# Performance work log

Hardware: AMD Instinct MI355X
Metric: run time of the kernel (lower is better)

Reference implementation:

```python
import jax, jax.numpy as jnp
import numpy as np

N = 50000
E = 800000
IN_FT = 256
OUT_FT = 64


def setup_inputs() -> dict:
    key = jax.random.key(0)
    k_seq, k_w, k_src, k_dst, k_val = jax.random.split(key, 5)
    seq = jax.random.normal(k_seq, (N, IN_FT), dtype=jnp.float32)
    # xavier_uniform_ for fc.weight [out_ft, in_ft]
    limit = float(np.sqrt(6.0 / (IN_FT + OUT_FT)))
    W = jax.random.uniform(k_w, (OUT_FT, IN_FT), minval=-limit, maxval=limit, dtype=jnp.float32)
    bias = jnp.zeros((OUT_FT,), dtype=jnp.float32)          # bias.data.fill_(0.0)
    alpha = jnp.full((1,), 0.25, dtype=jnp.float32)         # PReLU default init
    edge_src = jax.random.randint(k_src, (E,), 0, N, dtype=jnp.int32)
    edge_dst = jax.random.randint(k_dst, (E,), 0, N, dtype=jnp.int32)
    edge_val = jax.random.uniform(k_val, (E,), dtype=jnp.float32)
    return {"seq": seq, "W": W, "bias": bias, "alpha": alpha,
            "edge_src": edge_src, "edge_dst": edge_dst, "edge_val": edge_val}


def reference(seq, W, bias, alpha, edge_src, edge_dst, edge_val):
    # fc(seq): [N, in_ft] @ [in_ft, out_ft] -> [N, out_ft]
    fts = jnp.einsum('ni,oi->no', seq, W)
    # spmm(adj, fts): gather source features, scale by edge value, scatter-add to dst
    msgs = fts[edge_src] * edge_val[:, None]                # [E, out_ft]
    out = jax.ops.segment_sum(msgs, edge_dst, num_segments=seq.shape[0])
    out = out + bias
    # PReLU with scalar (single-channel) alpha
    return jnp.where(out >= 0, out, alpha * out)
```

## Files before the change

kernel.cpp:

```cpp
#include <hip/hip_runtime.h>
#include <hip/hip_fp16.h>

#define IN_FT 256
#define OUT_FT 64

constexpr int BIN_LOG   = 6;
constexpr int BIN_NODES = 1 << BIN_LOG;
constexpr int MAX_NBIN  = 1024;
constexpr int BIN_CAP   = 1536;
constexpr int SC_BLOCKS = 256;

constexpr float FXS  = 2097152.0f;
constexpr float IFXS = 1.0f / 2097152.0f;

typedef _Float16 half8 __attribute__((ext_vector_type(8)));
typedef float    f32x4 __attribute__((ext_vector_type(4)));

__global__ __launch_bounds__(256) void count_wconv(
    const float* __restrict__ W, half8* __restrict__ Wh,
    const int* __restrict__ dst, int* __restrict__ cnt, int E, int NBIN)
{
    const int t = (int)threadIdx.x;

    if ((int)blockIdx.x >= SC_BLOCKS) {
        int item = ((int)blockIdx.x - SC_BLOCKS) * 256 + t;
        int l  = item & 63;
        int kc = (item >> 6) & 7;
        int nt = item >> 9;
        int m  = l & 15;
        int q  = l >> 4;
        const float* wp = W + (size_t)(nt * 16 + m) * IN_FT + kc * 32 + q * 8;
        float4 w0 = *(const float4*)wp;
        float4 w1 = *(const float4*)(wp + 4);
        half8 hh;
        hh[0] = (_Float16)w0.x; hh[1] = (_Float16)w0.y;
        hh[2] = (_Float16)w0.z; hh[3] = (_Float16)w0.w;
        hh[4] = (_Float16)w1.x; hh[5] = (_Float16)w1.y;
        hh[6] = (_Float16)w1.z; hh[7] = (_Float16)w1.w;
        Wh[item] = hh;
        return;
    }

    __shared__ int h[MAX_NBIN];
    const int sb = (int)blockIdx.x;
    for (int i = t; i < NBIN; i += 256) h[i] = 0;
    __syncthreads();
    const int chunk = (E + SC_BLOCKS - 1) / SC_BLOCKS;
    const int s0 = sb * chunk;
    const int e0 = min(s0 + chunk, E);
    int i = s0 + t;
    for (; i + 768 < e0; i += 1024) {
        int d[4];
#pragma unroll
        for (int k = 0; k < 4; ++k) d[k] = dst[i + k * 256];
        __builtin_amdgcn_sched_barrier(0);
#pragma unroll
        for (int k = 0; k < 4; ++k) atomicAdd(&h[d[k] >> BIN_LOG], 1);
    }
    for (; i < e0; i += 256) atomicAdd(&h[dst[i] >> BIN_LOG], 1);
    __syncthreads();
    for (int b = t; b < NBIN; b += 256)
        cnt[(size_t)b * SC_BLOCKS + sb] = h[b];
}

__global__ __launch_bounds__(256) void scan_kernel(
    const int* __restrict__ cnt, int* __restrict__ offT,
    int* __restrict__ binTot)
{
    __shared__ int wsum[4];
    const int b    = (int)blockIdx.x;
    const int t    = (int)threadIdx.x;
    const int lane = t & 63;
    const int wv   = t >> 6;

    int c = cnt[(size_t)b * SC_BLOCKS + t];
    int incl = c;
#pragma unroll
    for (int d = 1; d < 64; d <<= 1) {
        int u = __shfl_up(incl, d, 64);
        if (lane >= d) incl += u;
    }
    if (lane == 63) wsum[wv] = incl;
    __syncthreads();
    int woff = 0;
#pragma unroll
    for (int w = 0; w < 4; ++w) if (w < wv) woff += wsum[w];
    int excl = woff + incl - c;
    offT[(size_t)t * MAX_NBIN + b] = excl;
    if (t == 255) binTot[b] = excl + c;
}

__global__ __launch_bounds__(256, 4) void fused_gemm_scatter(
    const float* __restrict__ seq, const half8* __restrict__ WhG,
    __half* __restrict__ fts, int N, int G,
    const int* __restrict__ src, const int* __restrict__ dst,
    const float* __restrict__ val, const int* __restrict__ offT,
    int2* __restrict__ binned, int E, int NBIN)
{
    __shared__ alignas(16) char smem[32768];
    const int t = (int)threadIdx.x;

    if ((int)blockIdx.x < SC_BLOCKS) {
        int* h = (int*)smem;
        const int sb = (int)blockIdx.x;
        for (int b = t; b < NBIN; b += 256)
            h[b] = offT[(size_t)sb * MAX_NBIN + b];
        __syncthreads();
        const int chunk = (E + SC_BLOCKS - 1) / SC_BLOCKS;
        const int s0 = sb * chunk;
        const int e0 = min(s0 + chunk, E);

        int i = s0 + t;
        for (; i + 768 < e0; i += 1024) {
            int d[4], s[4]; float v[4];
#pragma unroll
            for (int k = 0; k < 4; ++k) {
                d[k] = dst[i + k * 256];
                s[k] = src[i + k * 256];
                v[k] = val[i + k * 256];
            }
            __builtin_amdgcn_sched_barrier(0);
#pragma unroll
            for (int k = 0; k < 4; ++k) {
                int b = d[k] >> BIN_LOG;
                int pos = atomicAdd(&h[b], 1);
                if (pos < BIN_CAP) {
                    int2 pr;
                    pr.x = s[k] | ((d[k] & (BIN_NODES - 1)) << 16);
                    pr.y = __float_as_int(v[k] * FXS);
                    binned[(size_t)b * BIN_CAP + pos] = pr;
                }
            }
        }
        for (; i < e0; i += 256) {
            int d = dst[i];
            int b = d >> BIN_LOG;
            int pos = atomicAdd(&h[b], 1);
            if (pos < BIN_CAP) {
                int2 pr;
                pr.x = src[i] | ((d & (BIN_NODES - 1)) << 16);
                pr.y = __float_as_int(val[i] * FXS);
                binned[(size_t)b * BIN_CAP + pos] = pr;
            }
        }
        return;
    }

    const int wave = t >> 6;
    const int l    = t & 63;
    int nodeBase = ((int)blockIdx.x - SC_BLOCKS) * 64 + wave * 16;
    const bool active = (nodeBase < N);
    if (nodeBase > N - 16) nodeBase = N - 16;
    const int m = l & 15;
    const int q = l >> 4;
    const float* ap = seq + (size_t)(nodeBase + m) * IN_FT + q * 8;

    float4 A[16];
#pragma unroll
    for (int kc = 0; kc < 8; ++kc) {
        A[2 * kc]     = *(const float4*)(ap + kc * 32);
        A[2 * kc + 1] = *(const float4*)(ap + kc * 32 + 4);
    }
    {
        const int4* wg  = (const int4*)WhG;
        int4*       bsw = (int4*)smem;
#pragma unroll
        for (int i = 0; i < 8; ++i) bsw[i * 256 + t] = wg[i * 256 + t];
    }
    __syncthreads();
    const half8* Bs = (const half8*)smem;

    f32x4 acc0 = {0.f, 0.f, 0.f, 0.f};
    f32x4 acc1 = {0.f, 0.f, 0.f, 0.f};
    f32x4 acc2 = {0.f, 0.f, 0.f, 0.f};
    f32x4 acc3 = {0.f, 0.f, 0.f, 0.f};

#pragma unroll
    for (int kc = 0; kc < 8; ++kc) {
        float4 c0 = A[2 * kc], c1 = A[2 * kc + 1];
        half8 af;
        af[0] = (_Float16)c0.x; af[1] = (_Float16)c0.y;
        af[2] = (_Float16)c0.z; af[3] = (_Float16)c0.w;
        af[4] = (_Float16)c1.x; af[5] = (_Float16)c1.y;
        af[6] = (_Float16)c1.z; af[7] = (_Float16)c1.w;

        half8 b0 = Bs[(0 * 8 + kc) * 64 + l];
        half8 b1 = Bs[(1 * 8 + kc) * 64 + l];
        half8 b2 = Bs[(2 * 8 + kc) * 64 + l];
        half8 b3 = Bs[(3 * 8 + kc) * 64 + l];
        acc0 = __builtin_amdgcn_mfma_f32_16x16x32_f16(af, b0, acc0, 0, 0, 0);
        acc1 = __builtin_amdgcn_mfma_f32_16x16x32_f16(af, b1, acc1, 0, 0, 0);
        acc2 = __builtin_amdgcn_mfma_f32_16x16x32_f16(af, b2, acc2, 0, 0, 0);
        acc3 = __builtin_amdgcn_mfma_f32_16x16x32_f16(af, b3, acc3, 0, 0, 0);
    }

    if (active) {
#pragma unroll
        for (int r = 0; r < 4; ++r) {
            int node = nodeBase + q * 4 + r;
            __half* op = fts + (size_t)node * OUT_FT + m;
            op[0]  = __float2half(acc0[r]);
            op[16] = __float2half(acc1[r]);
            op[32] = __float2half(acc2[r]);
            op[48] = __float2half(acc3[r]);
        }
    }
}

__global__ __launch_bounds__(512, 4) void bin_reduce(
    const int2* __restrict__ binned, const int* __restrict__ binTot,
    const __half* __restrict__ fts, const float* __restrict__ bias,
    const float* __restrict__ alpha, float* __restrict__ out, int N)
{
    __shared__ int accum[BIN_NODES * OUT_FT];
    const int b    = (int)blockIdx.x;
    const int t    = (int)threadIdx.x;
    const int lane = t & 63;
    const int wv   = t >> 6;

    int4* a4 = (int4*)accum;
#pragma unroll
    for (int i = 0; i < (BIN_NODES * OUT_FT / 4) / 512; ++i)
        a4[i * 512 + t] = make_int4(0, 0, 0, 0);
    __syncthreads();

    const int nrec = min(binTot[b], BIN_CAP);
    const int2* rec = binned + (size_t)b * BIN_CAP;
    const unsigned short* ftsu = (const unsigned short*)fts + lane;

    int i = wv * 16;
    for (; i + 16 <= nrec; i += 8 * 16) {
        int2 pr[16];
#pragma unroll
        for (int k = 0; k < 16; ++k) pr[k] = rec[i + k];
        __builtin_amdgcn_sched_barrier(0);
        unsigned short h[16];
#pragma unroll
        for (int k = 0; k < 16; ++k)
            h[k] = ftsu[(size_t)(pr[k].x & 0xFFFF) * OUT_FT];
        __builtin_amdgcn_sched_barrier(0);
#pragma unroll
        for (int k = 0; k < 16; ++k) {
            float p = __half2float(__ushort_as_half(h[k])) * __int_as_float(pr[k].y);
            atomicAdd(&accum[(pr[k].x >> 16) * OUT_FT + lane], __float2int_rn(p));
        }
    }
    for (; i < nrec; ++i) {
        int2 pr = rec[i];
        float fv = __half2float(__ushort_as_half(ftsu[(size_t)(pr.x & 0xFFFF) * OUT_FT]));
        atomicAdd(&accum[(pr.x >> 16) * OUT_FT + lane],
                  __float2int_rn(fv * __int_as_float(pr.y)));
    }
    __syncthreads();

    const float a = alpha[0];
    for (int j = t; j < BIN_NODES * (OUT_FT / 4); j += 512) {
        int row  = j >> 4;
        int cc   = (j & 15) << 2;
        int node = (b << BIN_LOG) + row;
        if (node < N) {
            int4 v = *(int4*)&accum[row * OUT_FT + cc];
            float4 o;
            float x0 = (float)v.x * IFXS + bias[cc + 0];
            float x1 = (float)v.y * IFXS + bias[cc + 1];
            float x2 = (float)v.z * IFXS + bias[cc + 2];
            float x3 = (float)v.w * IFXS + bias[cc + 3];
            o.x = (x0 >= 0.f) ? x0 : a * x0;
            o.y = (x1 >= 0.f) ? x1 : a * x1;
            o.z = (x2 >= 0.f) ? x2 : a * x2;
            o.w = (x3 >= 0.f) ? x3 : a * x3;
            *(float4*)(out + (size_t)node * OUT_FT + cc) = o;
        }
    }
}

extern "C" void kernel_launch(void* const* d_in, const int* in_sizes, int n_in,
                              void* d_out, int out_size, void* d_ws, size_t ws_size,
                              hipStream_t stream) {
    const float* seq      = (const float*)d_in[0];
    const float* W        = (const float*)d_in[1];
    const float* bias     = (const float*)d_in[2];
    const float* alpha    = (const float*)d_in[3];
    const int*   edge_src = (const int*)d_in[4];
    const int*   edge_dst = (const int*)d_in[5];
    const float* edge_val = (const float*)d_in[6];
    float* out = (float*)d_out;

    const int N    = in_sizes[0] / IN_FT;
    const int E    = in_sizes[4];
    const int NBIN = (N + BIN_NODES - 1) >> BIN_LOG;

    size_t off = 0;
    auto take = [&](size_t bytes) -> char* {
        char* p = (char*)d_ws + off;
        off += (bytes + 255) & ~(size_t)255;
        return p;
    };
    __half* fts    = (__half*)take((size_t)N * OUT_FT * sizeof(__half));
    half8*  Wh     = (half8*)take((size_t)4 * 8 * 64 * sizeof(half8));
    int*    cnt    = (int*)take((size_t)NBIN * SC_BLOCKS * sizeof(int));
    int*    offT   = (int*)take((size_t)SC_BLOCKS * MAX_NBIN * sizeof(int));
    int*    binTot = (int*)take((size_t)NBIN * sizeof(int));
    int2*   binned = (int2*)take((size_t)NBIN * BIN_CAP * sizeof(int2));
    (void)ws_size;

    count_wconv<<<SC_BLOCKS + 8, 256, 0, stream>>>(W, Wh, edge_dst, cnt, E, NBIN);

    scan_kernel<<<NBIN, 256, 0, stream>>>(cnt, offT, binTot);

    const int G = (N + 63) / 64;
    fused_gemm_scatter<<<SC_BLOCKS + G, 256, 0, stream>>>(
        seq, Wh, fts, N, G, edge_src, edge_dst, edge_val,
        offT, binned, E, NBIN);

    bin_reduce<<<NBIN, 512, 0, stream>>>(
        binned, binTot, fts, bias, alpha, out, N);
}
```

Measured before the change: 157.4 us.

## Move GEMM into count kernel with multi-tile double-buffered loads

New measurement: 161.9 us. +2.9%, slower.

```diff
diff --git a/kernel.cpp b/kernel.cpp
--- a/kernel.cpp
+++ b/kernel.cpp
@@ -9,6 +9,7 @@
 constexpr int MAX_NBIN  = 1024;
 constexpr int BIN_CAP   = 1536;
 constexpr int SC_BLOCKS = 256;
+constexpr int TPB       = 4;
 
 constexpr float FXS  = 2097152.0f;
 constexpr float IFXS = 1.0f / 2097152.0f;
@@ -16,20 +17,45 @@
 typedef _Float16 half8 __attribute__((ext_vector_type(8)));
 typedef float    f32x4 __attribute__((ext_vector_type(4)));
 
-__global__ __launch_bounds__(256) void count_wconv(
-    const float* __restrict__ W, half8* __restrict__ Wh,
-    const int* __restrict__ dst, int* __restrict__ cnt, int E, int NBIN)
+__global__ __launch_bounds__(256, 4) void count_gemm(
+    const float* __restrict__ seq, const float* __restrict__ W,
+    __half* __restrict__ fts, const int* __restrict__ dst,
+    int* __restrict__ cnt, int N, int E, int NBIN, int TILES)
 {
+    __shared__ alignas(16) char smem[32768];
     const int t = (int)threadIdx.x;
 
-    if ((int)blockIdx.x >= SC_BLOCKS) {
-        int item = ((int)blockIdx.x - SC_BLOCKS) * 256 + t;
-        int l  = item & 63;
-        int kc = (item >> 6) & 7;
-        int nt = item >> 9;
-        int m  = l & 15;
-        int q  = l >> 4;
-        const float* wp = W + (size_t)(nt * 16 + m) * IN_FT + kc * 32 + q * 8;
+    if ((int)blockIdx.x < SC_BLOCKS) {
+        int* h = (int*)smem;
+        const int sb = (int)blockIdx.x;
+        for (int i = t; i < NBIN; i += 256) h[i] = 0;
+        __syncthreads();
+        const int chunk = (E + SC_BLOCKS - 1) / SC_BLOCKS;
+        const int s0 = sb * chunk;
+        const int e0 = min(s0 + chunk, E);
+        int i = s0 + t;
+        for (; i + 768 < e0; i += 1024) {
+            int d[4];
+#pragma unroll
+            for (int k = 0; k < 4; ++k) d[k] = dst[i + k * 256];
+            __builtin_amdgcn_sched_barrier(0);
+#pragma unroll
+            for (int k = 0; k < 4; ++k) atomicAdd(&h[d[k] >> BIN_LOG], 1);
+        }
+        for (; i < e0; i += 256) atomicAdd(&h[dst[i] >> BIN_LOG], 1);
+        __syncthreads();
+        for (int b = t; b < NBIN; b += 256)
+            cnt[(size_t)b * SC_BLOCKS + sb] = h[b];
+        return;
+    }
+
+    half8* Bs = (half8*)smem;
+#pragma unroll
+    for (int it = 0; it < 8; ++it) {
+        int item = it * 256 + t;
+        int l2 = item & 63, kc = (item >> 6) & 7, nt = item >> 9;
+        int mm = l2 & 15, qq = l2 >> 4;
+        const float* wp = W + (size_t)(nt * 16 + mm) * IN_FT + kc * 32 + qq * 8;
         float4 w0 = *(const float4*)wp;
         float4 w1 = *(const float4*)(wp + 4);
         half8 hh;
@@ -37,30 +63,111 @@
         hh[2] = (_Float16)w0.z; hh[3] = (_Float16)w0.w;
         hh[4] = (_Float16)w1.x; hh[5] = (_Float16)w1.y;
         hh[6] = (_Float16)w1.z; hh[7] = (_Float16)w1.w;
-        Wh[item] = hh;
-        return;
-    }
-
-    __shared__ int h[MAX_NBIN];
-    const int sb = (int)blockIdx.x;
-    for (int i = t; i < NBIN; i += 256) h[i] = 0;
-    __syncthreads();
-    const int chunk = (E + SC_BLOCKS - 1) / SC_BLOCKS;
-    const int s0 = sb * chunk;
-    const int e0 = min(s0 + chunk, E);
-    int i = s0 + t;
-    for (; i + 768 < e0; i += 1024) {
-        int d[4];
-#pragma unroll
-        for (int k = 0; k < 4; ++k) d[k] = dst[i + k * 256];
-        __builtin_amdgcn_sched_barrier(0);
-#pragma unroll
-        for (int k = 0; k < 4; ++k) atomicAdd(&h[d[k] >> BIN_LOG], 1);
-    }
-    for (; i < e0; i += 256) atomicAdd(&h[dst[i] >> BIN_LOG], 1);
-    __syncthreads();
-    for (int b = t; b < NBIN; b += 256)
-        cnt[(size_t)b * SC_BLOCKS + sb] = h[b];
+        Bs[item] = hh;
+    }
+    __syncthreads();
+
+    const int gb    = (int)blockIdx.x - SC_BLOCKS;
+    const int wv    = t >> 6;
+    const int l     = t & 63;
+    const int m     = l & 15;
+    const int q     = l >> 4;
+    const int tile0 = gb * TPB;
+    const int ntl   = min(TPB, TILES - tile0);
+    if (ntl <= 0) return;
+
+    f32x4 acc0 = {0.f,0.f,0.f,0.f}, acc1 = {0.f,0.f,0.f,0.f};
+    f32x4 acc2 = {0.f,0.f,0.f,0.f}, acc3 = {0.f,0.f,0.f,0.f};
+
+    auto issue = [&](float4* b, int s) {
+        const int tile = tile0 + (s >> 1);
+        const int hh = s & 1;
+        const float* ap = seq + (size_t)(tile * 64 + wv * 16 + m) * IN_FT
+                              + hh * 128 + q * 8;
+#pragma unroll
+        for (int kc = 0; kc < 4; ++kc) {
+            b[2 * kc]     = *(const float4*)(ap + kc * 32);
+            b[2 * kc + 1] = *(const float4*)(ap + kc * 32 + 4);
+        }
+    };
+    auto consume = [&](const float4* b, int hh) {
+#pragma unroll
+        for (int kc = 0; kc < 4; ++kc) {
+            float4 c0 = b[2 * kc], c1 = b[2 * kc + 1];
+            half8 af;
+            af[0] = (_Float16)c0.x; af[1] = (_Float16)c0.y;
+            af[2] = (_Float16)c0.z; af[3] = (_Float16)c0.w;
+            af[4] = (_Float16)c1.x; af[5] = (_Float16)c1.y;
+            af[6] = (_Float16)c1.z; af[7] = (_Float16)c1.w;
+            const int kg = hh * 4 + kc;
+            half8 b0 = Bs[(0 * 8 + kg) * 64 + l];
+            half8 b1 = Bs[(1 * 8 + kg) * 64 + l];
+            half8 b2 = Bs[(2 * 8 + kg) * 64 + l];
+            half8 b3 = Bs[(3 * 8 + kg) * 64 + l];
+            acc0 = __builtin_amdgcn_mfma_f32_16x16x32_f16(af, b0, acc0, 0, 0, 0);
+            acc1 = __builtin_amdgcn_mfma_f32_16x16x32_f16(af, b1, acc1, 0, 0, 0);
+            acc2 = __builtin_amdgcn_mfma_f32_16x16x32_f16(af, b2, acc2, 0, 0, 0);
+            acc3 = __builtin_amdgcn_mfma_f32_16x16x32_f16(af, b3, acc3, 0, 0, 0);
+        }
+    };
+    auto flush = [&](int ti) {
+        int nb = (tile0 + ti) * 64 + wv * 16;
+#pragma unroll
+        for (int r = 0; r < 4; ++r) {
+            int node = nb + q * 4 + r;
+            __half* op = fts + (size_t)node * OUT_FT + m;
+            op[0]  = __float2half(acc0[r]);
+            op[16] = __float2half(acc1[r]);
+            op[32] = __float2half(acc2[r]);
+            op[48] = __float2half(acc3[r]);
+        }
+        acc0 = (f32x4){0.f,0.f,0.f,0.f}; acc1 = (f32x4){0.f,0.f,0.f,0.f};
+        acc2 = (f32x4){0.f,0.f,0.f,0.f}; acc3 = (f32x4){0.f,0.f,0.f,0.f};
+    };
+
+    if (ntl == TPB) {
+        float4 bufA[8], bufB[8];
+        issue(bufA, 0);
+#pragma unroll
+        for (int s = 0; s < 2 * TPB; ++s) {
+            float4*       nxt = (s & 1) ? bufA : bufB;
+            const float4* cur = (s & 1) ? bufB : bufA;
+            if (s + 1 < 2 * TPB) issue(nxt, s + 1);
+            __builtin_amdgcn_sched_barrier(0);
+            asm volatile("" ::: "memory");
+            consume(cur, s & 1);
+            if (s & 1) flush(s >> 1);
+        }
+    } else {
+        for (int ti = 0; ti < ntl; ++ti) {
+            int tile = tile0 + ti;
+            int nb = tile * 64 + wv * 16;
+            const bool active = (nb < N);
+            if (nb > N - 16) nb = N - 16;
+            const float* ap = seq + (size_t)(nb + m) * IN_FT + q * 8;
+            float4 A[16];
+#pragma unroll
+            for (int kc = 0; kc < 8; ++kc) {
+                A[2 * kc]     = *(const float4*)(ap + kc * 32);
+                A[2 * kc + 1] = *(const float4*)(ap + kc * 32 + 4);
+            }
+            acc0 = (f32x4){0.f,0.f,0.f,0.f}; acc1 = (f32x4){0.f,0.f,0.f,0.f};
+            acc2 = (f32x4){0.f,0.f,0.f,0.f}; acc3 = (f32x4){0.f,0.f,0.f,0.f};
+#pragma unroll
+            for (int hh = 0; hh < 2; ++hh) consume(&A[hh * 8], hh);
+            if (active) {
+#pragma unroll
+                for (int r = 0; r < 4; ++r) {
+                    int node = nb + q * 4 + r;
+                    __half* op = fts + (size_t)node * OUT_FT + m;
+                    op[0]  = __float2half(acc0[r]);
+                    op[16] = __float2half(acc1[r]);
+                    op[32] = __float2half(acc2[r]);
+                    op[48] = __float2half(acc3[r]);
+                }
+            }
+        }
+    }
 }
 
 __global__ __launch_bounds__(256) void scan_kernel(
@@ -90,119 +197,52 @@
     if (t == 255) binTot[b] = excl + c;
 }
 
-__global__ __launch_bounds__(256, 4) void fused_gemm_scatter(
-    const float* __restrict__ seq, const half8* __restrict__ WhG,
-    __half* __restrict__ fts, int N, int G,
+__global__ __launch_bounds__(256) void place_kernel(
     const int* __restrict__ src, const int* __restrict__ dst,
     const float* __restrict__ val, const int* __restrict__ offT,
     int2* __restrict__ binned, int E, int NBIN)
 {
-    __shared__ alignas(16) char smem[32768];
-    const int t = (int)threadIdx.x;
-
-    if ((int)blockIdx.x < SC_BLOCKS) {
-        int* h = (int*)smem;
-        const int sb = (int)blockIdx.x;
-        for (int b = t; b < NBIN; b += 256)
-            h[b] = offT[(size_t)sb * MAX_NBIN + b];
-        __syncthreads();
-        const int chunk = (E + SC_BLOCKS - 1) / SC_BLOCKS;
-        const int s0 = sb * chunk;
-        const int e0 = min(s0 + chunk, E);
-
-        int i = s0 + t;
-        for (; i + 768 < e0; i += 1024) {
-            int d[4], s[4]; float v[4];
-#pragma unroll
-            for (int k = 0; k < 4; ++k) {
-                d[k] = dst[i + k * 256];
-                s[k] = src[i + k * 256];
-                v[k] = val[i + k * 256];
-            }
-            __builtin_amdgcn_sched_barrier(0);
-#pragma unroll
-            for (int k = 0; k < 4; ++k) {
-                int b = d[k] >> BIN_LOG;
-                int pos = atomicAdd(&h[b], 1);
-                if (pos < BIN_CAP) {
-                    int2 pr;
-                    pr.x = s[k] | ((d[k] & (BIN_NODES - 1)) << 16);
-                    pr.y = __float_as_int(v[k] * FXS);
-                    binned[(size_t)b * BIN_CAP + pos] = pr;
-                }
-            }
-        }
-        for (; i < e0; i += 256) {
-            int d = dst[i];
-            int b = d >> BIN_LOG;
+    __shared__ int h[MAX_NBIN];
+    const int t  = (int)threadIdx.x;
+    const int sb = (int)blockIdx.x;
+    for (int b = t; b < NBIN; b += 256)
+        h[b] = offT[(size_t)sb * MAX_NBIN + b];
+    __syncthreads();
+    const int chunk = (E + SC_BLOCKS - 1) / SC_BLOCKS;
+    const int s0 = sb * chunk;
+    const int e0 = min(s0 + chunk, E);
+
+    int i = s0 + t;
+    for (; i + 768 < e0; i += 1024) {
+        int d[4], s[4]; float v[4];
+#pragma unroll
+        for (int k = 0; k < 4; ++k) {
+            d[k] = dst[i + k * 256];
+            s[k] = src[i + k * 256];
+            v[k] = val[i + k * 256];
+        }
+        __builtin_amdgcn_sched_barrier(0);
+#pragma unroll
+        for (int k = 0; k < 4; ++k) {
+            int b = d[k] >> BIN_LOG;
             int pos = atomicAdd(&h[b], 1);
             if (pos < BIN_CAP) {
                 int2 pr;
-                pr.x = src[i] | ((d & (BIN_NODES - 1)) << 16);
-                pr.y = __float_as_int(val[i] * FXS);
+                pr.x = s[k] | ((d[k] & (BIN_NODES - 1)) << 16);
+                pr.y = __float_as_int(v[k] * FXS);
                 binned[(size_t)b * BIN_CAP + pos] = pr;
             }
         }
-        return;
-    }
-
-    const int wave = t >> 6;
-    const int l    = t & 63;
-    int nodeBase = ((int)blockIdx.x - SC_BLOCKS) * 64 + wave * 16;
-    const bool active = (nodeBase < N);
-    if (nodeBase > N - 16) nodeBase = N - 16;
-    const int m = l & 15;
-    const int q = l >> 4;
-    const float* ap = seq + (size_t)(nodeBase + m) * IN_FT + q * 8;
-
-    float4 A[16];
-#pragma unroll
-    for (int kc = 0; kc < 8; ++kc) {
-        A[2 * kc]     = *(const float4*)(ap + kc * 32);
-        A[2 * kc + 1] = *(const float4*)(ap + kc * 32 + 4);
-    }
-    {
-        const int4* wg  = (const int4*)WhG;
-        int4*       bsw = (int4*)smem;
-#pragma unroll
-        for (int i = 0; i < 8; ++i) bsw[i * 256 + t] = wg[i * 256 + t];
-    }
-    __syncthreads();
-    const half8* Bs = (const half8*)smem;
-
-    f32x4 acc0 = {0.f, 0.f, 0.f, 0.f};
-    f32x4 acc1 = {0.f, 0.f, 0.f, 0.f};
-    f32x4 acc2 = {0.f, 0.f, 0.f, 0.f};
-    f32x4 acc3 = {0.f, 0.f, 0.f, 0.f};
-
-#pragma unroll
-    for (int kc = 0; kc < 8; ++kc) {
-        float4 c0 = A[2 * kc], c1 = A[2 * kc + 1];
-        half8 af;
-        af[0] = (_Float16)c0.x; af[1] = (_Float16)c0.y;
-        af[2] = (_Float16)c0.z; af[3] = (_Float16)c0.w;
-        af[4] = (_Float16)c1.x; af[5] = (_Float16)c1.y;
-        af[6] = (_Float16)c1.z; af[7] = (_Float16)c1.w;
-
-        half8 b0 = Bs[(0 * 8 + kc) * 64 + l];
-        half8 b1 = Bs[(1 * 8 + kc) * 64 + l];
-        half8 b2 = Bs[(2 * 8 + kc) * 64 + l];
-        half8 b3 = Bs[(3 * 8 + kc) * 64 + l];
-        acc0 = __builtin_amdgcn_mfma_f32_16x16x32_f16(af, b0, acc0, 0, 0, 0);
-        acc1 = __builtin_amdgcn_mfma_f32_16x16x32_f16(af, b1, acc1, 0, 0, 0);
-        acc2 = __builtin_amdgcn_mfma_f32_16x16x32_f16(af, b2, acc2, 0, 0, 0);
-        acc3 = __builtin_amdgcn_mfma_f32_16x16x32_f16(af, b3, acc3, 0, 0, 0);
-    }
-
-    if (active) {
-#pragma unroll
-        for (int r = 0; r < 4; ++r) {
-            int node = nodeBase + q * 4 + r;
-            __half* op = fts + (size_t)node * OUT_FT + m;
-            op[0]  = __float2half(acc0[r]);
-            op[16] = __float2half(acc1[r]);
-            op[32] = __float2half(acc2[r]);
-            op[48] = __float2half(acc3[r]);
+    }
+    for (; i < e0; i += 256) {
+        int d = dst[i];
+        int b = d >> BIN_LOG;
+        int pos = atomicAdd(&h[b], 1);
+        if (pos < BIN_CAP) {
+            int2 pr;
+            pr.x = src[i] | ((d & (BIN_NODES - 1)) << 16);
+            pr.y = __float_as_int(val[i] * FXS);
+            binned[(size_t)b * BIN_CAP + pos] = pr;
         }
     }
 }
@@ -286,9 +326,11 @@
     const float* edge_val = (const float*)d_in[6];
     float* out = (float*)d_out;
 
-    const int N    = in_sizes[0] / IN_FT;
-    const int E    = in_sizes[4];
-    const int NBIN = (N + BIN_NODES - 1) >> BIN_LOG;
+    const int N     = in_sizes[0] / IN_FT;
+    const int E     = in_sizes[4];
+    const int NBIN  = (N + BIN_NODES - 1) >> BIN_LOG;
+    const int TILES = (N + 63) / 64;
+    const int GB    = (TILES + TPB - 1) / TPB;
 
     size_t off = 0;
     auto take = [&](size_t bytes) -> char* {
@@ -297,21 +339,19 @@
         return p;
     };
     __half* fts    = (__half*)take((size_t)N * OUT_FT * sizeof(__half));
-    half8*  Wh     = (half8*)take((size_t)4 * 8 * 64 * sizeof(half8));
     int*    cnt    = (int*)take((size_t)NBIN * SC_BLOCKS * sizeof(int));
     int*    offT   = (int*)take((size_t)SC_BLOCKS * MAX_NBIN * sizeof(int));
     int*    binTot = (int*)take((size_t)NBIN * sizeof(int));
     int2*   binned = (int2*)take((size_t)NBIN * BIN_CAP * sizeof(int2));
     (void)ws_size;
 
-    count_wconv<<<SC_BLOCKS + 8, 256, 0, stream>>>(W, Wh, edge_dst, cnt, E, NBIN);
+    count_gemm<<<SC_BLOCKS + GB, 256, 0, stream>>>(
+        seq, W, fts, edge_dst, cnt, N, E, NBIN, TILES);
 
     scan_kernel<<<NBIN, 256, 0, stream>>>(cnt, offT, binTot);
 
-    const int G = (N + 63) / 64;
-    fused_gemm_scatter<<<SC_BLOCKS + G, 256, 0, stream>>>(
-        seq, Wh, fts, N, G, edge_src, edge_dst, edge_val,
-        offT, binned, E, NBIN);
+    place_kernel<<<SC_BLOCKS, 256, 0, stream>>>(
+        edge_src, edge_dst, edge_val, offT, binned, E, NBIN);
 
     bin_reduce<<<NBIN, 512, 0, stream>>>(
         binned, binTot, fts, bias, alpha, out, N);
```
